# Kernel optimization log

Hardware: AMD Instinct MI355X
Metric: run time of the kernel (lower is better)

## Reference

```python
import jax, jax.numpy as jnp
import numpy as np
from jax import lax

H = 1024
W = 1024
WIN = 32
STR = 16
NH = (H - WIN) // STR + 1  # 63
N = NH * NH                # 3969 patches
DN3 = ('NCDHW', 'OIDHW', 'NCDHW')
DN2 = ('NCHW', 'OIHW', 'NCHW')


def setup_inputs() -> dict:
    key = jax.random.key(0)
    ks = jax.random.split(key, 13)
    r = lambda k, s, sc=0.05: jax.random.normal(k, s, dtype=jnp.float32) * sc
    return {
        'x1': jax.random.normal(ks[0], (1, 1, 1, H, W), jnp.float32),
        'x2': jax.random.normal(ks[1], (1, 1, 1, H, W), jnp.float32),
        'conv1_w': r(ks[2], (24, 1, 2, 8, 8)),      # Conv3d(1,24,(2,8,8)) [O,I,D,H,W]
        'conv1_b': r(ks[3], (24,)),
        'conv2_w': r(ks[4], (60, 24, 5, 5)),         # Conv2d(24,60,5)
        'conv2_b': r(ks[5], (60,)),
        'deconv2_w': r(ks[6], (60, 24, 5, 5)),       # ConvTranspose2d(60,24,5) [I,O,kH,kW]
        'deconv2_b': r(ks[7], (24,)),
        'deconv1_w': r(ks[8], (24, 1, 2, 8, 8)),     # ConvTranspose3d(24,1,(2,8,8)) [I,O,D,H,W]
        'deconv1_b': r(ks[9], (1,)),
        'lin_w': r(ks[10], (N, 2), 0.5),             # per-patch Linear(2,1) weights
        'lin_b': r(ks[11], (N,), 0.5),               # per-patch Linear(2,1) bias
        'linear1_w': r(ks[12], (1, 1), 0.5),         # Linear(1,1,bias=False)
    }


def _conv(x, w, b, dn):
    nd = w.ndim - 2
    y = lax.conv_general_dilated(x, w, (1,) * nd, 'VALID', dimension_numbers=dn)
    return y + b.reshape((1, -1) + (1,) * nd)


def _convT(x, w, b, dn):
    # stride-1, pad-0 transposed conv == full-pad conv with flipped, IO-swapped kernel
    nd = w.ndim - 2
    wf = jnp.flip(w, axis=tuple(range(2, w.ndim))).swapaxes(0, 1)  # [O,I,*k]
    pad = [(k - 1, k - 1) for k in w.shape[2:]]
    y = lax.conv_general_dilated(x, wf, (1,) * nd, pad, dimension_numbers=dn)
    return y + b.reshape((1, -1) + (1,) * nd)


def reference(x1, x2, conv1_w, conv1_b, conv2_w, conv2_b, deconv2_w, deconv2_b,
              deconv1_w, deconv1_b, lin_w, lin_b, linear1_w):
    x = jnp.concatenate([x1, x2], axis=2)[0, 0]  # [2,H,W]
    idx = (jnp.arange(NH) * STR)[:, None] + jnp.arange(WIN)[None, :]  # [NH,32]
    # unfold dims 3,4 with window 32 / stride 16 -> [2,NH,NW,32,32]
    patches = x[:, idx[:, None, :, None], idx[None, :, None, :]]
    outX = patches.reshape(2, N, WIN, WIN).transpose(1, 0, 2, 3)[:, None]  # [N,1,2,32,32]
    h = jax.nn.elu(_conv(outX, conv1_w, conv1_b, DN3))        # [N,24,1,25,25]
    h = jax.nn.relu(_conv(h[:, :, 0], conv2_w, conv2_b, DN2))  # [N,60,21,21]
    h = jax.nn.elu(_convT(h, deconv2_w, deconv2_b, DN2))       # [N,24,25,25]
    h = _convT(h[:, :, None], deconv1_w, deconv1_b, DN3)       # [N,1,2,32,32]
    # per-patch Linear(2,1) over depth channels, batched over all patches
    p = jnp.einsum('nchw,nc->nhw', h[:, 0], lin_w) + lin_b[:, None, None]  # [N,32,32]
    p = p.reshape(NH, NH, WIN, WIN)
    # col2im: overlap-add fold, block 32, stride 16 -> [H,W]
    recon = jnp.zeros((H, W), jnp.float32).at[idx[:, None, :, None], idx[None, :, None, :]].add(p)
    outX2 = recon * linear1_w[0, 0]  # Linear(1,1,bias=False) per pixel
    return x2 - outX2.reshape(x2.shape)
```

## Files before the change

### kernel.cpp

```cpp
#include <hip/hip_runtime.h>
#include <hip/hip_bf16.h>

static constexpr int H_ = 1024;
static constexpr int W_ = 1024;
static constexpr int STR_ = 16;
static constexpr int NH_ = 63;
static constexpr int NPATCH_ = NH_ * NH_;

typedef short bf16x8 __attribute__((ext_vector_type(8)));
typedef short short4v __attribute__((ext_vector_type(4)));
typedef float f32x4 __attribute__((ext_vector_type(4)));

static constexpr int SH1_STRIDE = 48;
static constexpr int SH2_BASE   = 30016;
static constexpr int SH2_STRIDE = 120;
static constexpr int ZROW_REL   = 441 * SH2_STRIDE;
static constexpr int SPB0       = 30016;
static constexpr int SPB1       = 35136;
static constexpr int SWC_BASE   = 30016;
static constexpr int SP_ACC     = 34112;
static constexpr int LDS_BYTES  = 83072;

__device__ __forceinline__ unsigned short f2bf(float x) {
    __hip_bfloat16 b = __float2bfloat16(x);
    return __builtin_bit_cast(unsigned short, b);
}

__device__ __forceinline__ f32x4 mfma_bf16(bf16x8 a, bf16x8 b, f32x4 c) {
    return __builtin_amdgcn_mfma_f32_16x16x32_bf16(a, b, c, 0, 0, 0);
}

__device__ __forceinline__ float elu_neg(float x) { return __expf(x) - 1.f; }

__global__ __launch_bounds__(1024, 4) void fused_patch_kernel(
    const float* __restrict__ x1, const float* __restrict__ x2,
    const float* __restrict__ c1b, const float* __restrict__ c2b,
    const float* __restrict__ d2b, const float* __restrict__ d1b,
    const float* __restrict__ lin_w, const float* __restrict__ lin_b,
    const unsigned short* __restrict__ w1frag,
    const unsigned short* __restrict__ w2frag,
    const unsigned short* __restrict__ dw2frag,
    const float* __restrict__ dw1,
    float* __restrict__ recon)
{
    __shared__ alignas(16) char sbuf[LDS_BYTES];
    const int n  = blockIdx.x;
    const int t  = (int)threadIdx.x;
    const int pi = n / NH_, pj = n % NH_;
    const int Y0 = pi * STR_, X0 = pj * STR_;
    const int wv = t >> 6, lane = t & 63;
    const int ln15 = lane & 15, quad = lane >> 4;

    bf16x8 w1b[8];
    #pragma unroll
    for (int g = 0; g < 8; ++g)
        w1b[g] = *(const bf16x8*)(w1frag + (g * 64 + lane) * 8);
    const float lw0  = lin_w[2 * n], lw1 = lin_w[2 * n + 1];
    const float lbn  = lin_b[n];
    const float d1b0 = d1b[0];
    const float c1b0 = c1b[ln15];
    const float c1b1 = (16 + ln15 < 24) ? c1b[16 + ln15] : 0.f;
    float c2bias[4];
    #pragma unroll
    for (int nt = 0; nt < 4; ++nt) {
        int o = nt * 16 + ln15;
        c2bias[nt] = (o < 60) ? c2b[o] : 0.f;
    }
    const float db0 = d2b[ln15];
    const float db1 = (16 + ln15 < 24) ? d2b[16 + ln15] : 0.f;
    float dwp[4] = {0.f, 0.f, 0.f, 0.f};
    {
        int r0 = t >> 5, c0 = t & 31;
        if (c0 < 24) {
            dwp[0] = dw1[(c0 * 2 + 0) * 64 + r0];
            dwp[1] = dw1[(c0 * 2 + 1) * 64 + r0];
        }
        int k1 = t + 1024, r1 = k1 >> 5, c1 = k1 & 31;
        if (c1 < 24) {
            dwp[2] = dw1[(c1 * 2 + 0) * 64 + r1];
            dwp[3] = dw1[(c1 * 2 + 1) * 64 + r1];
        }
    }

    if (t < 30)      ((float*)(sbuf + SH2_BASE + ZROW_REL))[t] = 0.f;
    else if (t < 34) ((float*)(sbuf + 30000))[t - 30] = 0.f;
    else if (t < 38) ((float*)(sbuf + SH2_BASE + 53040))[t - 34] = 0.f;
    for (int k = t; k < 2048; k += 1024) {
        int d = k >> 10, r = k & 1023, y = r >> 5, x = r & 31;
        unsigned short b = f2bf((d ? x2 : x1)[(Y0 + y) * W_ + (X0 + x)]);
        int row = (d * 32 + y) * 40;
        ((unsigned short*)(sbuf + SPB0))[row + x] = b;
        if (x > 0) ((unsigned short*)(sbuf + SPB1))[row + x - 1] = b;
    }
    __syncthreads();

    for (int tl = wv; tl < 50; tl += 16) {
        const int vcol = tl >> 1, ubase = (tl & 1) * 16;
        const int u = ubase + ln15;
        const char* abase = sbuf + ((vcol & 1) ? SPB1 : SPB0) + (vcol & ~1) * 2;
        f32x4 acc[2];
        acc[0] = (f32x4){0.f, 0.f, 0.f, 0.f};
        acc[1] = (f32x4){0.f, 0.f, 0.f, 0.f};
        #pragma unroll
        for (int kc = 0; kc < 4; ++kc) {
            const int idx8 = kc * 4 + quad;
            const int dd = idx8 >> 3, pp = idx8 & 7;
            const unsigned int* ap = (const unsigned int*)(abase + (dd * 32 + u + pp) * 80);
            union { unsigned int u4[4]; bf16x8 v; } af;
            af.u4[0] = ap[0]; af.u4[1] = ap[1]; af.u4[2] = ap[2]; af.u4[3] = ap[3];
            acc[0] = mfma_bf16(af.v, w1b[kc * 2 + 0], acc[0]);
            acc[1] = mfma_bf16(af.v, w1b[kc * 2 + 1], acc[1]);
        }
        #pragma unroll
        for (int ntp = 0; ntp < 2; ++ntp) {
            const int c = ntp * 16 + ln15;
            if (c < 24) {
                const float bias = ntp ? c1b1 : c1b0;
                #pragma unroll
                for (int r = 0; r < 4; ++r) {
                    int uu = ubase + quad * 4 + r;
                    if (uu < 25) {
                        float hv = acc[ntp][r] + bias;
                        hv = hv > 0.f ? hv : elu_neg(hv);
                        *(unsigned short*)(sbuf + (uu * 25 + vcol) * SH1_STRIDE + c * 2) = f2bf(hv);
                    }
                }
            }
        }
    }
    __syncthreads();

    if (wv < 14) {
        int abase2[2];
        #pragma unroll
        for (int i = 0; i < 2; ++i) {
            int m = (wv + i * 14) * 16 + ln15;
            if (m > 440) m = 440;
            abase2[i] = ((m / 21) * 25 + (m % 21)) * SH1_STRIDE;
        }
        f32x4 acc2[2][4];
        #pragma unroll
        for (int i = 0; i < 2; ++i)
            #pragma unroll
            for (int nt = 0; nt < 4; ++nt)
                acc2[i][nt] = (f32x4){0.f, 0.f, 0.f, 0.f};

        const unsigned short* wb = w2frag + lane * 8;
        bf16x8 bcur[4], acur[2];
        #pragma unroll
        for (int nt = 0; nt < 4; ++nt)
            bcur[nt] = *(const bf16x8*)(wb + nt * 512);
        #pragma unroll
        for (int i = 0; i < 2; ++i)
            acur[i] = *(const bf16x8*)(sbuf + abase2[i] + quad * 16);

        #pragma unroll
        for (int tap = 0; tap < 25; ++tap) {
            bf16x8 bnxt[4], anxt[2];
            if (tap < 24) {
                const int toff1 = (((tap + 1) / 5) * 25 + ((tap + 1) % 5)) * SH1_STRIDE;
                #pragma unroll
                for (int nt = 0; nt < 4; ++nt)
                    bnxt[nt] = *(const bf16x8*)(wb + ((tap + 1) * 4 + nt) * 512);
                #pragma unroll
                for (int i = 0; i < 2; ++i)
                    anxt[i] = *(const bf16x8*)(sbuf + abase2[i] + toff1 + quad * 16);
            }
            #pragma unroll
            for (int i = 0; i < 2; ++i)
                #pragma unroll
                for (int nt = 0; nt < 4; ++nt)
                    acc2[i][nt] = mfma_bf16(acur[i], bcur[nt], acc2[i][nt]);
            if (tap < 24) {
                #pragma unroll
                for (int nt = 0; nt < 4; ++nt) bcur[nt] = bnxt[nt];
                acur[0] = anxt[0]; acur[1] = anxt[1];
            }
        }
        #pragma unroll
        for (int i = 0; i < 2; ++i) {
            #pragma unroll
            for (int r = 0; r < 4; ++r) {
                int pix = (wv + i * 14) * 16 + quad * 4 + r;
                if (pix < 441) {
                    unsigned short* rowp = (unsigned short*)(sbuf + SH2_BASE + pix * SH2_STRIDE);
                    #pragma unroll
                    for (int nt = 0; nt < 4; ++nt) {
                        int o = nt * 16 + ln15;
                        if (o < 60)
                            rowp[o] = f2bf(fmaxf(acc2[i][nt][r] + c2bias[nt], 0.f));
                    }
                }
            }
        }
    }
    __syncthreads();

    f32x4 acc3[3][2];
    {
        #pragma unroll
        for (int i = 0; i < 3; ++i) {
            acc3[i][0] = (f32x4){0.f, 0.f, 0.f, 0.f};
            acc3[i][1] = (f32x4){0.f, 0.f, 0.f, 0.f};
        }
        int uarr[3], varr[3], a120[3];
        bool mval[3];
        #pragma unroll
        for (int i = 0; i < 3; ++i) {
            int m = (wv + i * 16) * 16 + ln15;
            mval[i] = (m < 625);
            int mc = mval[i] ? m : 0;
            uarr[i] = mc / 25; varr[i] = mc % 25;
            a120[i] = (uarr[i] * 21 + varr[i]) * SH2_STRIDE;
        }
        const unsigned short* db = dw2frag + lane * 8;
        bf16x8 bc[4];
        #pragma unroll
        for (int f = 0; f < 4; ++f)
            bc[f] = *(const bf16x8*)(db + f * 512);
        #pragma unroll
        for (int tap = 0; tap < 25; ++tap) {
            const int dy = tap / 5, dx = tap % 5;
            const int t2off = (dy * 21 + dx) * SH2_STRIDE;
            bf16x8 bn[4];
            if (tap < 24) {
                #pragma unroll
                for (int f = 0; f < 4; ++f)
                    bn[f] = *(const bf16x8*)(db + ((tap + 1) * 4 + f) * 512);
            }
            #pragma unroll
            for (int i = 0; i < 3; ++i) {
                if (i == 2 && wv >= 8) continue;
                int yv = uarr[i] - dy, xv = varr[i] - dx;
                bool ok = mval[i] && ((unsigned)yv < 21u) && ((unsigned)xv < 21u);
                int ra = ok ? (a120[i] - t2off) : ZROW_REL;
                const char* ap = sbuf + SH2_BASE + ra + quad * 16;
                short4v lo0 = *(const short4v*)(ap);
                short4v hi0 = *(const short4v*)(ap + 8);
                bf16x8 a0 = __builtin_shufflevector(lo0, hi0, 0, 1, 2, 3, 4, 5, 6, 7);
                acc3[i][0] = mfma_bf16(a0, bc[0], acc3[i][0]);
                acc3[i][1] = mfma_bf16(a0, bc[1], acc3[i][1]);
                short4v lo1 = *(const short4v*)(ap + 64);
                short4v hi1 = *(const short4v*)(ap + 72);
                bf16x8 a1 = __builtin_shufflevector(lo1, hi1, 0, 1, 2, 3, 4, 5, 6, 7);
                acc3[i][0] = mfma_bf16(a1, bc[2], acc3[i][0]);
                acc3[i][1] = mfma_bf16(a1, bc[3], acc3[i][1]);
            }
            if (tap < 24) {
                bc[0] = bn[0]; bc[1] = bn[1]; bc[2] = bn[2]; bc[3] = bn[3];
            }
        }
    }
    __syncthreads();

    float* sp = (float*)(sbuf + SP_ACC);
    {
        const int c1ok = (16 + ln15 < 24);
        #pragma unroll
        for (int i = 0; i < 3; ++i) {
            if (i == 2 && wv >= 8) continue;
            #pragma unroll
            for (int r = 0; r < 4; ++r) {
                int pix = (wv + i * 16) * 16 + quad * 4 + r;
                if (pix < 625) {
                    unsigned short* rowp = (unsigned short*)(sbuf + pix * SH1_STRIDE);
                    float hv = acc3[i][0][r] + db0;
                    rowp[ln15] = f2bf(hv > 0.f ? hv : elu_neg(hv));
                    if (c1ok) {
                        float hw = acc3[i][1][r] + db1;
                        rowp[16 + ln15] = f2bf(hw > 0.f ? hw : elu_neg(hw));
                    }
                }
            }
        }
    }
    {
        int r0 = t >> 5, c0 = t & 31;
        ((unsigned short*)(sbuf + SWC_BASE))[r0 * 32 + c0] = f2bf(lw0 * dwp[0] + lw1 * dwp[1]);
        int k1 = t + 1024, r1 = k1 >> 5, c1 = k1 & 31;
        ((unsigned short*)(sbuf + SWC_BASE))[r1 * 32 + c1] = f2bf(lw0 * dwp[2] + lw1 * dwp[3]);
    }
    sp[t] = 0.f;
    __syncthreads();

    {
        bf16x8 wbv[4];
        #pragma unroll
        for (int nt = 0; nt < 4; ++nt)
            wbv[nt] = *(const bf16x8*)(sbuf + SWC_BASE + (nt * 16 + ln15) * 64 + quad * 16);
        #pragma unroll
        for (int i = 0; i < 3; ++i) {
            int mt = wv + i * 16;
            if (mt >= 40) continue;
            int m = mt * 16 + ln15;
            if (m > 624) m = 624;
            bf16x8 a = *(const bf16x8*)(sbuf + m * SH1_STRIDE + quad * 16);
            #pragma unroll
            for (int nt = 0; nt < 4; ++nt) {
                f32x4 acc4 = (f32x4){0.f, 0.f, 0.f, 0.f};
                acc4 = mfma_bf16(a, wbv[nt], acc4);
                #pragma unroll
                for (int r = 0; r < 4; ++r) {
                    int pix = mt * 16 + quad * 4 + r;
                    if (pix < 625) {
                        int u = pix / 25, v = pix % 25;
                        int rv = nt * 16 + ln15;
                        atomicAdd(&sp[(u + (rv >> 3)) * 32 + v + (rv & 7)], acc4[r]);
                    }
                }
            }
        }
    }
    __syncthreads();

    const float obias = d1b0 * (lw0 + lw1) + lbn;
    {
        int yy = t >> 5, xx = t & 31;
        atomicAdd(&recon[(Y0 + yy) * W_ + (X0 + xx)], sp[t] + obias);
    }
}

__global__ void prep_kernel(const float* __restrict__ c1w,
                            const float* __restrict__ c2w,
                            const float* __restrict__ d2w,
                            unsigned short* __restrict__ w1frag,
                            unsigned short* __restrict__ w2frag,
                            unsigned short* __restrict__ dw2frag)
{
    int i = blockIdx.x * blockDim.x + threadIdx.x;
    if (i < 51200) {
        int j = i & 7, lane = (i >> 3) & 63;
        int ln15 = lane & 15, quad = lane >> 4;
        if (i < 4096) {
            int g = i >> 9;
            int kc = g >> 1, nt = g & 1;
            int nn = nt * 16 + ln15, k = kc * 32 + quad * 8 + j;
            w1frag[i] = f2bf((nn < 24) ? c1w[nn * 128 + k] : 0.f);
        }
        {
            int nt = (i >> 9) & 3, tap = i >> 11;
            int o = nt * 16 + ln15, c = quad * 8 + j;
            float v = (o < 60 && c < 24) ? c2w[(o * 24 + c) * 25 + tap] : 0.f;
            w2frag[i] = f2bf(v);
        }
        {
            int nt = (i >> 9) & 1, kc = (i >> 10) & 1, tap = i >> 11;
            int k = kc * 32 + quad * 8 + j, c = nt * 16 + ln15;
            float v = (k < 60 && c < 24) ? d2w[(k * 24 + c) * 25 + tap] : 0.f;
            dw2frag[i] = f2bf(v);
        }
    }
}

__global__ void finalize_kernel(const float* __restrict__ x2,
                                const float* __restrict__ l1w,
                                float* __restrict__ out)
{
    int i = blockIdx.x * blockDim.x + threadIdx.x;
    if (i < H_ * W_) {
        float r = out[i];
        out[i] = x2[i] - r * l1w[0];
    }
}

extern "C" void kernel_launch(void* const* d_in, const int* in_sizes, int n_in,
                              void* d_out, int out_size, void* d_ws, size_t ws_size,
                              hipStream_t stream)
{
    const float* x1  = (const float*)d_in[0];
    const float* x2  = (const float*)d_in[1];
    const float* c1w = (const float*)d_in[2];
    const float* c1b = (const float*)d_in[3];
    const float* c2w = (const float*)d_in[4];
    const float* c2b = (const float*)d_in[5];
    const float* d2w = (const float*)d_in[6];
    const float* d2b = (const float*)d_in[7];
    const float* d1w = (const float*)d_in[8];
    const float* d1b = (const float*)d_in[9];
    const float* lw  = (const float*)d_in[10];
    const float* lb  = (const float*)d_in[11];
    const float* l1w = (const float*)d_in[12];

    float*          out     = (float*)d_out;
    unsigned short* w1frag  = (unsigned short*)d_ws;
    unsigned short* w2frag  = (unsigned short*)((char*)d_ws + 8192);
    unsigned short* dw2frag = (unsigned short*)((char*)d_ws + 110592);

    hipMemsetAsync(d_out, 0, (size_t)H_ * W_ * sizeof(float), stream);
    prep_kernel<<<100, 512, 0, stream>>>(c1w, c2w, d2w, w1frag, w2frag, dw2frag);
    fused_patch_kernel<<<NPATCH_, 1024, 0, stream>>>(x1, x2, c1b, c2b, d2b, d1b,
                                                     lw, lb, w1frag, w2frag, dw2frag,
                                                     d1w, out);
    finalize_kernel<<<(H_ * W_ + 255) / 256, 256, 0, stream>>>(x2, l1w, out);
}
```

Baseline: 1.385 ms.

## Process two horizontally adjacent patches per block, sharing overlapping conv1 output

Each block now handles a pair of neighbouring patches in a row, loading a 32x48 input strip and computing conv1 once over a 25x41 region. That region holds both patches' conv1 outputs, so the overlapping columns are computed once instead of twice. Later stages (conv2, deconv2, deconv1 plus the per-patch linear) run over both patches using doubled LDS buffers, and the block count drops by about half. LDS use rises to about 155 KB per block, which cuts blocks resident per CU, and the last column of blocks does redundant work on a single patch.

```diff
diff --git a/kernel.cpp b/kernel.cpp
--- a/kernel.cpp
+++ b/kernel.cpp
@@ -6,20 +6,25 @@
 static constexpr int STR_ = 16;
 static constexpr int NH_ = 63;
 static constexpr int NPATCH_ = NH_ * NH_;
+static constexpr int NGRP_ = 32;
+static constexpr int NBLK_ = NH_ * NGRP_;
 
 typedef short bf16x8 __attribute__((ext_vector_type(8)));
 typedef short short4v __attribute__((ext_vector_type(4)));
 typedef float f32x4 __attribute__((ext_vector_type(4)));
 
-static constexpr int SH1_STRIDE = 48;
-static constexpr int SH2_BASE   = 30016;
-static constexpr int SH2_STRIDE = 120;
-static constexpr int ZROW_REL   = 441 * SH2_STRIDE;
-static constexpr int SPB0       = 30016;
-static constexpr int SPB1       = 35136;
-static constexpr int SWC_BASE   = 30016;
-static constexpr int SP_ACC     = 34112;
-static constexpr int LDS_BYTES  = 83072;
+static constexpr int GAP16   = 49200;
+static constexpr int CP0     = 49216;
+static constexpr int CP1     = 55360;
+static constexpr int SH2_0   = 49216;
+static constexpr int SH2SZ   = 52920;
+static constexpr int SH2_1   = SH2_0 + SH2SZ;
+static constexpr int ZROW    = 155056;
+static constexpr int H3SZ    = 30000;
+static constexpr int SWC0    = 60000;
+static constexpr int SWC1    = 64096;
+static constexpr int SPA     = 68192;
+static constexpr int LDS_BYTES = 155200;
 
 __device__ __forceinline__ unsigned short f2bf(float x) {
     __hip_bfloat16 b = __float2bfloat16(x);
@@ -44,19 +49,24 @@
     float* __restrict__ recon)
 {
     __shared__ alignas(16) char sbuf[LDS_BYTES];
-    const int n  = blockIdx.x;
-    const int t  = (int)threadIdx.x;
-    const int pi = n / NH_, pj = n % NH_;
-    const int Y0 = pi * STR_, X0 = pj * STR_;
-    const int wv = t >> 6, lane = t & 63;
+    const int b   = blockIdx.x;
+    const int pi  = b / NGRP_, g = b - pi * NGRP_;
+    const int pj0 = 2 * g;
+    const int npat = (pj0 + 1 < NH_) ? 2 : 1;
+    const int n0  = pi * NH_ + pj0;
+    const int n1  = (npat == 2) ? (n0 + 1) : n0;
+    const int Y0  = pi * STR_, X0 = pj0 * STR_;
+    const int t   = (int)threadIdx.x;
+    const int wv  = t >> 6, lane = t & 63;
     const int ln15 = lane & 15, quad = lane >> 4;
 
     bf16x8 w1b[8];
     #pragma unroll
-    for (int g = 0; g < 8; ++g)
-        w1b[g] = *(const bf16x8*)(w1frag + (g * 64 + lane) * 8);
-    const float lw0  = lin_w[2 * n], lw1 = lin_w[2 * n + 1];
-    const float lbn  = lin_b[n];
+    for (int gg = 0; gg < 8; ++gg)
+        w1b[gg] = *(const bf16x8*)(w1frag + (gg * 64 + lane) * 8);
+    const float lw00 = lin_w[2 * n0], lw01 = lin_w[2 * n0 + 1];
+    const float lw10 = lin_w[2 * n1], lw11 = lin_w[2 * n1 + 1];
+    const float lbn0 = lin_b[n0], lbn1 = lin_b[n1];
     const float d1b0 = d1b[0];
     const float c1b0 = c1b[ln15];
     const float c1b1 = (16 + ln15 < 24) ? c1b[16 + ln15] : 0.f;
@@ -82,22 +92,28 @@
         }
     }
 
-    if (t < 30)      ((float*)(sbuf + SH2_BASE + ZROW_REL))[t] = 0.f;
-    else if (t < 34) ((float*)(sbuf + 30000))[t - 30] = 0.f;
-    else if (t < 38) ((float*)(sbuf + SH2_BASE + 53040))[t - 34] = 0.f;
-    for (int k = t; k < 2048; k += 1024) {
-        int d = k >> 10, r = k & 1023, y = r >> 5, x = r & 31;
-        unsigned short b = f2bf((d ? x2 : x1)[(Y0 + y) * W_ + (X0 + x)]);
-        int row = (d * 32 + y) * 40;
-        ((unsigned short*)(sbuf + SPB0))[row + x] = b;
-        if (x > 0) ((unsigned short*)(sbuf + SPB1))[row + x - 1] = b;
-    }
-    __syncthreads();
-
-    for (int tl = wv; tl < 50; tl += 16) {
-        const int vcol = tl >> 1, ubase = (tl & 1) * 16;
-        const int u = ubase + ln15;
-        const char* abase = sbuf + ((vcol & 1) ? SPB1 : SPB0) + (vcol & ~1) * 2;
+    if (t < 4)       ((float*)(sbuf + GAP16))[t] = 0.f;
+    else if (t < 8)  ((float*)(sbuf + SH2_1))[t - 4] = 0.f;
+    else if (t < 42) ((float*)(sbuf + ZROW))[t - 8] = 0.f;
+    #pragma unroll
+    for (int it = 0; it < 3; ++it) {
+        int k = t + it * 1024;
+        int d = (k >= 1536) ? 1 : 0;
+        int rem = k - d * 1536;
+        int y = rem / 48, x = rem - y * 48;
+        int xg = X0 + x; if (xg > W_ - 1) xg = W_ - 1;
+        unsigned short bb = f2bf((d ? x2 : x1)[(Y0 + y) * W_ + xg]);
+        int row = (d * 32 + y) * 48;
+        ((unsigned short*)(sbuf + CP0))[row + x] = bb;
+        if (x > 0) ((unsigned short*)(sbuf + CP1))[row + x - 1] = bb;
+    }
+    __syncthreads();
+
+    for (int tl = wv; tl < 65; tl += 16) {
+        int m = tl * 16 + ln15; if (m > 1024) m = 1024;
+        int u = m / 41, v = m - u * 41;
+        const char* cps = sbuf + ((v & 1) ? CP1 : CP0);
+        const int vb2 = (v & ~1) * 2;
         f32x4 acc[2];
         acc[0] = (f32x4){0.f, 0.f, 0.f, 0.f};
         acc[1] = (f32x4){0.f, 0.f, 0.f, 0.f};
@@ -105,11 +121,11 @@
         for (int kc = 0; kc < 4; ++kc) {
             const int idx8 = kc * 4 + quad;
             const int dd = idx8 >> 3, pp = idx8 & 7;
-            const unsigned int* ap = (const unsigned int*)(abase + (dd * 32 + u + pp) * 80);
-            union { unsigned int u4[4]; bf16x8 v; } af;
+            const unsigned int* ap = (const unsigned int*)(cps + (dd * 32 + u + pp) * 96 + vb2);
+            union { unsigned int u4[4]; bf16x8 v8; } af;
             af.u4[0] = ap[0]; af.u4[1] = ap[1]; af.u4[2] = ap[2]; af.u4[3] = ap[3];
-            acc[0] = mfma_bf16(af.v, w1b[kc * 2 + 0], acc[0]);
-            acc[1] = mfma_bf16(af.v, w1b[kc * 2 + 1], acc[1]);
+            acc[0] = mfma_bf16(af.v8, w1b[kc * 2 + 0], acc[0]);
+            acc[1] = mfma_bf16(af.v8, w1b[kc * 2 + 1], acc[1]);
         }
         #pragma unroll
         for (int ntp = 0; ntp < 2; ++ntp) {
@@ -118,11 +134,11 @@
                 const float bias = ntp ? c1b1 : c1b0;
                 #pragma unroll
                 for (int r = 0; r < 4; ++r) {
-                    int uu = ubase + quad * 4 + r;
-                    if (uu < 25) {
+                    int mm = tl * 16 + quad * 4 + r;
+                    if (mm < 1025) {
                         float hv = acc[ntp][r] + bias;
                         hv = hv > 0.f ? hv : elu_neg(hv);
-                        *(unsigned short*)(sbuf + (uu * 25 + vcol) * SH1_STRIDE + c * 2) = f2bf(hv);
+                        *(unsigned short*)(sbuf + mm * 48 + c * 2) = f2bf(hv);
                     }
                 }
             }
@@ -130,13 +146,18 @@
     }
     __syncthreads();
 
-    if (wv < 14) {
-        int abase2[2];
+    auto s2pass = [&](int t0, int t1) {
+        const bool h1 = (t1 < 56);
+        int ab[2], loc[2], Pp[2];
         #pragma unroll
         for (int i = 0; i < 2; ++i) {
-            int m = (wv + i * 14) * 16 + ln15;
-            if (m > 440) m = 440;
-            abase2[i] = ((m / 21) * 25 + (m % 21)) * SH1_STRIDE;
+            int tt = i ? (h1 ? t1 : t0) : t0;
+            int P = (tt >= 28) ? 1 : 0;
+            int lc = tt - P * 28;
+            int mm = lc * 16 + ln15; if (mm > 440) mm = 440;
+            int y = mm / 21, x = mm - y * 21;
+            ab[i] = (y * 41 + P * 16 + x) * 48;
+            loc[i] = lc; Pp[i] = P;
         }
         f32x4 acc2[2][4];
         #pragma unroll
@@ -144,46 +165,40 @@
             #pragma unroll
             for (int nt = 0; nt < 4; ++nt)
                 acc2[i][nt] = (f32x4){0.f, 0.f, 0.f, 0.f};
-
         const unsigned short* wb = w2frag + lane * 8;
-        bf16x8 bcur[4], acur[2];
-        #pragma unroll
-        for (int nt = 0; nt < 4; ++nt)
-            bcur[nt] = *(const bf16x8*)(wb + nt * 512);
-        #pragma unroll
-        for (int i = 0; i < 2; ++i)
-            acur[i] = *(const bf16x8*)(sbuf + abase2[i] + quad * 16);
-
-        #pragma unroll
-        for (int tap = 0; tap < 25; ++tap) {
-            bf16x8 bnxt[4], anxt[2];
-            if (tap < 24) {
-                const int toff1 = (((tap + 1) / 5) * 25 + ((tap + 1) % 5)) * SH1_STRIDE;
+        #pragma unroll
+        for (int p = 0; p < 5; ++p) {
+            #pragma unroll
+            for (int q = 0; q < 5; ++q) {
+                const int tap  = p * 5 + q;
+                const int toff = (p * 41 + q) * 48;
+                bf16x8 bfr[4];
                 #pragma unroll
                 for (int nt = 0; nt < 4; ++nt)
-                    bnxt[nt] = *(const bf16x8*)(wb + ((tap + 1) * 4 + nt) * 512);
-                #pragma unroll
-                for (int i = 0; i < 2; ++i)
-                    anxt[i] = *(const bf16x8*)(sbuf + abase2[i] + toff1 + quad * 16);
-            }
-            #pragma unroll
-            for (int i = 0; i < 2; ++i)
-                #pragma unroll
-                for (int nt = 0; nt < 4; ++nt)
-                    acc2[i][nt] = mfma_bf16(acur[i], bcur[nt], acc2[i][nt]);
-            if (tap < 24) {
-                #pragma unroll
-                for (int nt = 0; nt < 4; ++nt) bcur[nt] = bnxt[nt];
-                acur[0] = anxt[0]; acur[1] = anxt[1];
+                    bfr[nt] = *(const bf16x8*)(wb + (tap * 4 + nt) * 512);
+                {
+                    bf16x8 a = *(const bf16x8*)(sbuf + ab[0] + toff + quad * 16);
+                    #pragma unroll
+                    for (int nt = 0; nt < 4; ++nt)
+                        acc2[0][nt] = mfma_bf16(a, bfr[nt], acc2[0][nt]);
+                }
+                if (h1) {
+                    bf16x8 a = *(const bf16x8*)(sbuf + ab[1] + toff + quad * 16);
+                    #pragma unroll
+                    for (int nt = 0; nt < 4; ++nt)
+                        acc2[1][nt] = mfma_bf16(a, bfr[nt], acc2[1][nt]);
+                }
             }
         }
         #pragma unroll
         for (int i = 0; i < 2; ++i) {
+            if (i == 1 && !h1) continue;
+            unsigned short* base = (unsigned short*)(sbuf + SH2_0 + Pp[i] * SH2SZ);
             #pragma unroll
             for (int r = 0; r < 4; ++r) {
-                int pix = (wv + i * 14) * 16 + quad * 4 + r;
+                int pix = loc[i] * 16 + quad * 4 + r;
                 if (pix < 441) {
-                    unsigned short* rowp = (unsigned short*)(sbuf + SH2_BASE + pix * SH2_STRIDE);
+                    unsigned short* rowp = base + pix * 60;
                     #pragma unroll
                     for (int nt = 0; nt < 4; ++nt) {
                         int o = nt * 16 + ln15;
@@ -193,77 +208,77 @@
                 }
             }
         }
-    }
-    __syncthreads();
-
-    f32x4 acc3[3][2];
-    {
-        #pragma unroll
-        for (int i = 0; i < 3; ++i) {
+    };
+    s2pass(wv, wv + 16);
+    s2pass(wv + 32, wv + 48);
+    __syncthreads();
+
+    f32x4 acc3[5][2];
+    {
+        #pragma unroll
+        for (int i = 0; i < 5; ++i) {
             acc3[i][0] = (f32x4){0.f, 0.f, 0.f, 0.f};
             acc3[i][1] = (f32x4){0.f, 0.f, 0.f, 0.f};
         }
-        int uarr[3], varr[3], a120[3];
-        bool mval[3];
-        #pragma unroll
-        for (int i = 0; i < 3; ++i) {
-            int m = (wv + i * 16) * 16 + ln15;
+        int uarr[5], varr[5], aoff[5];
+        bool mval[5];
+        #pragma unroll
+        for (int i = 0; i < 5; ++i) {
+            int t5 = wv + 16 * i;
+            int P = (t5 >= 40) ? 1 : 0;
+            int lc = t5 - P * 40;
+            int m = lc * 16 + ln15;
             mval[i] = (m < 625);
             int mc = mval[i] ? m : 0;
-            uarr[i] = mc / 25; varr[i] = mc % 25;
-            a120[i] = (uarr[i] * 21 + varr[i]) * SH2_STRIDE;
+            uarr[i] = mc / 25; varr[i] = mc - uarr[i] * 25;
+            aoff[i] = SH2_0 + P * SH2SZ + (uarr[i] * 21 + varr[i]) * 120;
         }
         const unsigned short* db = dw2frag + lane * 8;
-        bf16x8 bc[4];
-        #pragma unroll
-        for (int f = 0; f < 4; ++f)
-            bc[f] = *(const bf16x8*)(db + f * 512);
-        #pragma unroll
-        for (int tap = 0; tap < 25; ++tap) {
-            const int dy = tap / 5, dx = tap % 5;
-            const int t2off = (dy * 21 + dx) * SH2_STRIDE;
-            bf16x8 bn[4];
-            if (tap < 24) {
+        #pragma unroll
+        for (int dy = 0; dy < 5; ++dy) {
+            #pragma unroll
+            for (int dx = 0; dx < 5; ++dx) {
+                const int tap = dy * 5 + dx;
+                const int t2o = (dy * 21 + dx) * 120;
+                bf16x8 bc0 = *(const bf16x8*)(db + tap * 2048);
+                bf16x8 bc1 = *(const bf16x8*)(db + tap * 2048 + 512);
+                bf16x8 bc2 = *(const bf16x8*)(db + tap * 2048 + 1024);
+                bf16x8 bc3 = *(const bf16x8*)(db + tap * 2048 + 1536);
                 #pragma unroll
-                for (int f = 0; f < 4; ++f)
-                    bn[f] = *(const bf16x8*)(db + ((tap + 1) * 4 + f) * 512);
-            }
-            #pragma unroll
-            for (int i = 0; i < 3; ++i) {
-                if (i == 2 && wv >= 8) continue;
-                int yv = uarr[i] - dy, xv = varr[i] - dx;
-                bool ok = mval[i] && ((unsigned)yv < 21u) && ((unsigned)xv < 21u);
-                int ra = ok ? (a120[i] - t2off) : ZROW_REL;
-                const char* ap = sbuf + SH2_BASE + ra + quad * 16;
-                short4v lo0 = *(const short4v*)(ap);
-                short4v hi0 = *(const short4v*)(ap + 8);
-                bf16x8 a0 = __builtin_shufflevector(lo0, hi0, 0, 1, 2, 3, 4, 5, 6, 7);
-                acc3[i][0] = mfma_bf16(a0, bc[0], acc3[i][0]);
-                acc3[i][1] = mfma_bf16(a0, bc[1], acc3[i][1]);
-                short4v lo1 = *(const short4v*)(ap + 64);
-                short4v hi1 = *(const short4v*)(ap + 72);
-                bf16x8 a1 = __builtin_shufflevector(lo1, hi1, 0, 1, 2, 3, 4, 5, 6, 7);
-                acc3[i][0] = mfma_bf16(a1, bc[2], acc3[i][0]);
-                acc3[i][1] = mfma_bf16(a1, bc[3], acc3[i][1]);
-            }
-            if (tap < 24) {
-                bc[0] = bn[0]; bc[1] = bn[1]; bc[2] = bn[2]; bc[3] = bn[3];
-            }
-        }
-    }
-    __syncthreads();
-
-    float* sp = (float*)(sbuf + SP_ACC);
+                for (int i = 0; i < 5; ++i) {
+                    int yv = uarr[i] - dy, xv = varr[i] - dx;
+                    bool ok = mval[i] && ((unsigned)yv < 21u) && ((unsigned)xv < 21u);
+                    int ra = ok ? (aoff[i] - t2o) : ZROW;
+                    const char* ap = sbuf + ra + quad * 16;
+                    short4v lo0 = *(const short4v*)(ap);
+                    short4v hi0 = *(const short4v*)(ap + 8);
+                    bf16x8 a0 = __builtin_shufflevector(lo0, hi0, 0, 1, 2, 3, 4, 5, 6, 7);
+                    acc3[i][0] = mfma_bf16(a0, bc0, acc3[i][0]);
+                    acc3[i][1] = mfma_bf16(a0, bc1, acc3[i][1]);
+                    short4v lo1 = *(const short4v*)(ap + 64);
+                    short4v hi1 = *(const short4v*)(ap + 72);
+                    bf16x8 a1 = __builtin_shufflevector(lo1, hi1, 0, 1, 2, 3, 4, 5, 6, 7);
+                    acc3[i][0] = mfma_bf16(a1, bc2, acc3[i][0]);
+                    acc3[i][1] = mfma_bf16(a1, bc3, acc3[i][1]);
+                }
+            }
+        }
+    }
+    __syncthreads();
+
+    float* sp = (float*)(sbuf + SPA);
     {
         const int c1ok = (16 + ln15 < 24);
         #pragma unroll
-        for (int i = 0; i < 3; ++i) {
-            if (i == 2 && wv >= 8) continue;
+        for (int i = 0; i < 5; ++i) {
+            int t5 = wv + 16 * i;
+            int P = (t5 >= 40) ? 1 : 0;
+            int lc = t5 - P * 40;
             #pragma unroll
             for (int r = 0; r < 4; ++r) {
-                int pix = (wv + i * 16) * 16 + quad * 4 + r;
+                int pix = lc * 16 + quad * 4 + r;
                 if (pix < 625) {
-                    unsigned short* rowp = (unsigned short*)(sbuf + pix * SH1_STRIDE);
+                    unsigned short* rowp = (unsigned short*)(sbuf + P * H3SZ + pix * 48);
                     float hv = acc3[i][0][r] + db0;
                     rowp[ln15] = f2bf(hv > 0.f ? hv : elu_neg(hv));
                     if (c1ok) {
@@ -276,47 +291,65 @@
     }
     {
         int r0 = t >> 5, c0 = t & 31;
-        ((unsigned short*)(sbuf + SWC_BASE))[r0 * 32 + c0] = f2bf(lw0 * dwp[0] + lw1 * dwp[1]);
+        ((unsigned short*)(sbuf + SWC0))[r0 * 32 + c0] = f2bf(lw00 * dwp[0] + lw01 * dwp[1]);
+        ((unsigned short*)(sbuf + SWC1))[r0 * 32 + c0] = f2bf(lw10 * dwp[0] + lw11 * dwp[1]);
         int k1 = t + 1024, r1 = k1 >> 5, c1 = k1 & 31;
-        ((unsigned short*)(sbuf + SWC_BASE))[r1 * 32 + c1] = f2bf(lw0 * dwp[2] + lw1 * dwp[3]);
-    }
-    sp[t] = 0.f;
-    __syncthreads();
-
-    {
-        bf16x8 wbv[4];
-        #pragma unroll
-        for (int nt = 0; nt < 4; ++nt)
-            wbv[nt] = *(const bf16x8*)(sbuf + SWC_BASE + (nt * 16 + ln15) * 64 + quad * 16);
-        #pragma unroll
-        for (int i = 0; i < 3; ++i) {
-            int mt = wv + i * 16;
-            if (mt >= 40) continue;
-            int m = mt * 16 + ln15;
-            if (m > 624) m = 624;
-            bf16x8 a = *(const bf16x8*)(sbuf + m * SH1_STRIDE + quad * 16);
+        ((unsigned short*)(sbuf + SWC0))[r1 * 32 + c1] = f2bf(lw00 * dwp[2] + lw01 * dwp[3]);
+        ((unsigned short*)(sbuf + SWC1))[r1 * 32 + c1] = f2bf(lw10 * dwp[2] + lw11 * dwp[3]);
+    }
+    sp[t] = 0.f; sp[t + 1024] = 0.f;
+    __syncthreads();
+
+    {
+        int ntoff[4];
+        #pragma unroll
+        for (int nt = 0; nt < 4; ++nt) {
+            int rv = nt * 16 + ln15;
+            ntoff[nt] = (rv >> 3) * 32 + (rv & 7);
+        }
+        #pragma unroll
+        for (int i = 0; i < 5; ++i) {
+            int t5 = wv + 16 * i;
+            int P = (t5 >= 40) ? 1 : 0;
+            int lc = t5 - P * 40;
+            int m = lc * 16 + ln15; if (m > 624) m = 624;
+            bf16x8 a = *(const bf16x8*)(sbuf + P * H3SZ + m * 48 + quad * 16);
+            const char* swc = sbuf + (P ? SWC1 : SWC0);
+            bf16x8 wbv[4];
+            #pragma unroll
+            for (int nt = 0; nt < 4; ++nt)
+                wbv[nt] = *(const bf16x8*)(swc + (nt * 16 + ln15) * 64 + quad * 16);
+            float* spP = sp + P * 1024;
+            int uvb[4]; bool pok[4];
+            #pragma unroll
+            for (int r = 0; r < 4; ++r) {
+                int pix = lc * 16 + quad * 4 + r;
+                pok[r] = (pix < 625);
+                int pc = pok[r] ? pix : 0;
+                uvb[r] = (pc / 25) * 32 + (pc % 25);
+            }
             #pragma unroll
             for (int nt = 0; nt < 4; ++nt) {
                 f32x4 acc4 = (f32x4){0.f, 0.f, 0.f, 0.f};
                 acc4 = mfma_bf16(a, wbv[nt], acc4);
                 #pragma unroll
                 for (int r = 0; r < 4; ++r) {
-                    int pix = mt * 16 + quad * 4 + r;
-                    if (pix < 625) {
-                        int u = pix / 25, v = pix % 25;
-                        int rv = nt * 16 + ln15;
-                        atomicAdd(&sp[(u + (rv >> 3)) * 32 + v + (rv & 7)], acc4[r]);
-                    }
-                }
-            }
-        }
-    }
-    __syncthreads();
-
-    const float obias = d1b0 * (lw0 + lw1) + lbn;
+                    if (pok[r])
+                        atomicAdd(&spP[uvb[r] + ntoff[nt]], acc4[r]);
+                }
+            }
+        }
+    }
+    __syncthreads();
+
     {
         int yy = t >> 5, xx = t & 31;
-        atomicAdd(&recon[(Y0 + yy) * W_ + (X0 + xx)], sp[t] + obias);
+        float ob0 = d1b0 * (lw00 + lw01) + lbn0;
+        atomicAdd(&recon[(Y0 + yy) * W_ + X0 + xx], sp[t] + ob0);
+        if (npat == 2) {
+            float ob1 = d1b0 * (lw10 + lw11) + lbn1;
+            atomicAdd(&recon[(Y0 + yy) * W_ + X0 + 16 + xx], sp[t + 1024] + ob1);
+        }
     }
 }
 
@@ -388,8 +421,8 @@
 
     hipMemsetAsync(d_out, 0, (size_t)H_ * W_ * sizeof(float), stream);
     prep_kernel<<<100, 512, 0, stream>>>(c1w, c2w, d2w, w1frag, w2frag, dw2frag);
-    fused_patch_kernel<<<NPATCH_, 1024, 0, stream>>>(x1, x2, c1b, c2b, d2b, d1b,
-                                                     lw, lb, w1frag, w2frag, dw2frag,
-                                                     d1w, out);
+    fused_patch_kernel<<<NBLK_, 1024, 0, stream>>>(x1, x2, c1b, c2b, d2b, d1b,
+                                                   lw, lb, w1frag, w2frag, dw2frag,
+                                                   d1w, out);
     finalize_kernel<<<(H_ * W_ + 255) / 256, 256, 0, stream>>>(x2, l1w, out);
 }
```

New measurement: 1.396 ms. Within noise of the previous version (+0.8%).
